# Performance work log

Measured on AMD Instinct MI355X. Metric: run time of the kernel, lower is better.

The kernel has to match this reference:

```python
import jax, jax.numpy as jnp
import numpy as np

B, HW, C = 32, 56, 128
WS, SS, NH = 7, 3, 4
HD = C // NH
SCALE = HD ** -0.5
NWIN = (HW // WS) ** 2  # 64 windows per image
N = WS * WS             # 49 tokens per window


def _build_constants():
    # relative position index [N, N] into flattened (13*13) bias table
    coords = np.stack(np.meshgrid(np.arange(WS), np.arange(WS), indexing='ij'))  # [2,7,7]
    cf = coords.reshape(2, -1)                       # [2,49]
    rel = cf[:, :, None] - cf[:, None, :]            # [2,49,49]
    rel = rel.transpose(1, 2, 0).copy()              # [49,49,2]
    rel[:, :, 0] += WS - 1
    rel[:, :, 1] += WS - 1
    rel[:, :, 0] *= 2 * WS - 1
    pos_index = rel.sum(-1)                          # [49,49]
    # shifted-window attention mask [nW, N, N]
    img = np.zeros((HW, HW))
    sl = (slice(0, -WS), slice(-WS, -SS), slice(-SS, None))
    cnt = 0
    for h in sl:
        for w in sl:
            img[h, w] = cnt
            cnt += 1
    mw = img.reshape(HW // WS, WS, HW // WS, WS).transpose(0, 2, 1, 3).reshape(NWIN, N)
    am = mw[:, None, :] - mw[:, :, None]             # unsqueeze(1) - unsqueeze(2)
    am = np.where(am != 0, -100.0, 0.0).astype(np.float32)
    return jnp.asarray(pos_index), jnp.asarray(am)

POS_INDEX, ATTN_MASK = _build_constants()


def _ln(x, w, b, eps=1e-5):
    mu = x.mean(-1, keepdims=True)
    var = ((x - mu) ** 2).mean(-1, keepdims=True)
    return (x - mu) * jax.lax.rsqrt(var + eps) * w + b


def setup_inputs() -> dict:
    key = jax.random.key(0)
    ks = jax.random.split(key, 10)
    s = 0.02
    return {
        'x': jax.random.normal(ks[0], (B, HW * HW, C), jnp.float32),
        'norm1_w': jnp.ones((C,), jnp.float32),
        'norm1_b': jnp.zeros((C,), jnp.float32),
        'qkv_w': jax.random.normal(ks[1], (C, 3 * C), jnp.float32) * s,
        'qkv_b': jax.random.normal(ks[2], (3 * C,), jnp.float32) * s,
        'proj_w': jax.random.normal(ks[3], (C, C), jnp.float32) * s,
        'proj_b': jax.random.normal(ks[4], (C,), jnp.float32) * s,
        'pos_bias_table': jax.random.normal(ks[5], (2 * WS - 1, 2 * WS - 1, NH), jnp.float32) * s,
        'mlp_w1': jax.random.normal(ks[6], (C, 4 * C), jnp.float32) * s,
        'mlp_b1': jnp.zeros((4 * C,), jnp.float32),
        'mlp_w2': jax.random.normal(ks[7], (4 * C, C), jnp.float32) * s,
        'mlp_b2': jnp.zeros((C,), jnp.float32),
        'norm2_w': jnp.ones((C,), jnp.float32),
        'norm2_b': jnp.zeros((C,), jnp.float32),
    }


def reference(x, norm1_w, norm1_b, qkv_w, qkv_b, proj_w, proj_b, pos_bias_table,
              mlp_w1, mlp_b1, mlp_w2, mlp_b2, norm2_w, norm2_b):
    G = HW // WS  # grid of windows per side
    Bw = B * NWIN
    shortcut = x
    y = _ln(x, norm1_w, norm1_b).reshape(B, HW, HW, C)
    # cyclic shift
    y = jnp.roll(y, (-SS, -SS), axis=(1, 2))
    # window partition -> [B*nW, 49, C]
    yw = y.reshape(B, G, WS, G, WS, C).transpose(0, 1, 3, 2, 4, 5).reshape(Bw, N, C)
    # qkv projection
    qkv = (yw @ qkv_w + qkv_b).reshape(Bw, N, 3, NH, HD).transpose(2, 0, 3, 1, 4)
    q, k, v = qkv[0] * SCALE, qkv[1], qkv[2]  # [Bw, NH, N, HD]
    attn = jnp.einsum('bhnd,bhmd->bhnm', q, k)
    # relative position bias [NH, N, N]
    bias = pos_bias_table.reshape(-1, NH)[POS_INDEX]  # [N,N,NH]
    attn = attn + bias.transpose(2, 0, 1)[None]
    # shift mask per window
    attn = attn.reshape(B, NWIN, NH, N, N) + ATTN_MASK[None, :, None]
    attn = jax.nn.softmax(attn.reshape(Bw, NH, N, N), axis=-1)
    out = jnp.einsum('bhnm,bhmd->bhnd', attn, v).transpose(0, 2, 1, 3).reshape(Bw, N, C)
    out = out @ proj_w + proj_b
    # window reverse
    out = out.reshape(B, G, G, WS, WS, C).transpose(0, 1, 3, 2, 4, 5).reshape(B, HW, HW, C)
    out = jnp.roll(out, (SS, SS), axis=(1, 2)).reshape(B, HW * HW, C)
    x = shortcut + out
    h = _ln(x, norm2_w, norm2_b)
    h = jax.nn.gelu(h @ mlp_w1 + mlp_b1, approximate=False) @ mlp_w2 + mlp_b2
    return x + h
```

## Files before the change

kernel.cpp:

```cpp
#include <hip/hip_runtime.h>
#include <hip/hip_bf16.h>

#define NTOK 100352
#define SCALE_Q 0.17677669529663687f

typedef __bf16 bf16x8 __attribute__((ext_vector_type(8)));
typedef float f32x4 __attribute__((ext_vector_type(4)));
struct bf2 { __hip_bfloat16 x, y; };
struct __align__(8) bh4 { __hip_bfloat16 a, b, c, d; };

__device__ __forceinline__ int wt_to_tok(int wt) {
  int w = wt / 49, n = wt - w * 49;
  int b = w >> 6, wi = w & 63;
  int gh = wi >> 3, gw = wi & 7;
  int r = n / 7, c = n - r * 7;
  int hs = gh * 7 + r + 3; if (hs >= 56) hs -= 56;
  int ws = gw * 7 + c + 3; if (ws >= 56) ws -= 56;
  return (b * 56 + hs) * 56 + ws;
}

__device__ __forceinline__ float gelu_fast(float v) {
  float y = 0.7978845608028654f * (v + 0.044715f * v * v * v);
  float ay = fabsf(y);
  float e = __expf(-2.0f * ay);
  float t = (1.0f - e) / (1.0f + e);
  t = copysignf(t, y);
  return 0.5f * v * (1.0f + t);
}

__global__ __launch_bounds__(256) void prep_all(const float* __restrict__ qkvw,
                                                const float* __restrict__ projw,
                                                const float* __restrict__ w1,
                                                const float* __restrict__ w2,
                                                __hip_bfloat16* __restrict__ dst) {
  int i = blockIdx.x * 256 + threadIdx.x;
  float v;
  if (i < 49152) { int n = i >> 7, k = i & 127; v = qkvw[k * 384 + n]; }
  else if (i < 65536) { int j = i - 49152; int n = j >> 7, k = j & 127; v = projw[k * 128 + n]; }
  else if (i < 131072) { int j = i - 65536; int n = j >> 7, k = j & 127; v = w1[k * 512 + n]; }
  else { int j = i - 131072; int n = j / 512, k = j - n * 512; v = w2[k * 128 + n]; }
  dst[i] = __float2bfloat16(v);
}

__global__ __launch_bounds__(256) void ln1_apply(const float* __restrict__ x,
                                                 const float* __restrict__ nw,
                                                 const float* __restrict__ nb,
                                                 __hip_bfloat16* __restrict__ xn) {
  int wt = blockIdx.x * 4 + (threadIdx.x >> 6);
  int lane = threadIdx.x & 63;
  int tok = wt_to_tok(wt);
  float2 v = *(const float2*)(x + (size_t)tok * 128 + lane * 2);
  float s = v.x + v.y, ss = v.x * v.x + v.y * v.y;
#pragma unroll
  for (int off = 32; off; off >>= 1) {
    s += __shfl_xor(s, off);
    ss += __shfl_xor(ss, off);
  }
  float mu = s * (1.0f / 128.0f);
  float rstd = rsqrtf(ss * (1.0f / 128.0f) - mu * mu + 1e-5f);
  float2 wv = *(const float2*)(nw + lane * 2);
  float2 bv = *(const float2*)(nb + lane * 2);
  bf2 o;
  o.x = __float2bfloat16((v.x - mu) * rstd * wv.x + bv.x);
  o.y = __float2bfloat16((v.y - mu) * rstd * wv.y + bv.y);
  *(bf2*)(xn + (size_t)wt * 128 + lane * 2) = o;
}

__global__ __launch_bounds__(256) void attn_mfma(const __hip_bfloat16* __restrict__ qkv,
                                                 const float* __restrict__ ptab,
                                                 __hip_bfloat16* __restrict__ attnout) {
  __shared__ __align__(16) char lds[4 * 12288];
  const int tid = threadIdx.x;
  const int lane = tid & 63, h = tid >> 6;
  const int w = blockIdx.x;
  const int wi = w & 63, gh = wi >> 3, gw = wi & 7;
  char* Pl = lds + h * 12288;
  char* VTl = Pl + 8192;
  const int lxi = lane & 15, lq = lane >> 4, lg4 = (lane >> 4) * 4;

  const __hip_bfloat16* base = qkv + (size_t)w * 49 * 384 + h * 32;
  __hip_bfloat16* op = attnout + (size_t)w * 49 * 128 + h * 32;

  bf16x8 qa[4], kb[4];
#pragma unroll
  for (int mi = 0; mi < 4; ++mi) {
    int t = mi * 16 + lxi; if (t > 48) t = 48;
    qa[mi] = *(const bf16x8*)(base + (size_t)t * 384 + lq * 8);
    kb[mi] = *(const bf16x8*)(base + (size_t)t * 384 + 128 + lq * 8);
  }
  {
    union { bf16x8 v; __hip_bfloat16 e[8]; } vv[4];
    const __hip_bfloat16* vp = base + (size_t)(lane < 49 ? lane : 0) * 384 + 256;
#pragma unroll
    for (int q = 0; q < 4; ++q) vv[q].v = *(const bf16x8*)(vp + q * 8);
    __hip_bfloat16 z = __float2bfloat16(0.0f);
#pragma unroll
    for (int q = 0; q < 4; ++q)
#pragma unroll
      for (int e = 0; e < 8; ++e) {
        int d = q * 8 + e;
        __hip_bfloat16 val = (lane < 49) ? vv[q].e[e] : z;
        *(__hip_bfloat16*)(VTl + d * 128 + ((lane * 2) ^ ((d & 7) << 4))) = val;
      }
  }

  f32x4 s[4][4] = {};
#pragma unroll
  for (int mi = 0; mi < 4; ++mi)
#pragma unroll
    for (int ni = 0; ni < 4; ++ni)
      s[mi][ni] = __builtin_amdgcn_mfma_f32_16x16x32_bf16(qa[mi], kb[ni], s[mi][ni], 0, 0, 0);

  int rj[4], cj[4], cntj[4], jbad[4];
#pragma unroll
  for (int ni = 0; ni < 4; ++ni) {
    int jc = ni * 16 + lxi;
    jbad[ni] = (jc > 48);
    int jj = jbad[ni] ? 48 : jc;
    rj[ni] = jj / 7; cj[ni] = jj - rj[ni] * 7;
    int hj = gh * 7 + rj[ni], wj = gw * 7 + cj[ni];
    cntj[ni] = (hj < 49 ? 0 : (hj < 53 ? 3 : 6)) + (wj < 49 ? 0 : (wj < 53 ? 1 : 2));
  }
#pragma unroll
  for (int mi = 0; mi < 4; ++mi)
#pragma unroll
    for (int j = 0; j < 4; ++j) {
      int i = mi * 16 + lg4 + j; if (i > 48) i = 48;
      int ri = i / 7, ci = i - ri * 7;
      int hi_ = gh * 7 + ri, wi_ = gw * 7 + ci;
      int cnti = (hi_ < 49 ? 0 : (hi_ < 53 ? 3 : 6)) + (wi_ < 49 ? 0 : (wi_ < 53 ? 1 : 2));
#pragma unroll
      for (int ni = 0; ni < 4; ++ni) {
        float b = ptab[((ri - rj[ni] + 6) * 13 + (ci - cj[ni] + 6)) * 4 + h];
        float val = s[mi][ni][j] * SCALE_Q + b;
        if (cnti != cntj[ni]) val -= 100.0f;
        if (jbad[ni]) val = -1e30f;
        s[mi][ni][j] = val;
      }
    }

#pragma unroll
  for (int mi = 0; mi < 4; ++mi)
#pragma unroll
    for (int j = 0; j < 4; ++j) {
      float m = fmaxf(fmaxf(s[mi][0][j], s[mi][1][j]), fmaxf(s[mi][2][j], s[mi][3][j]));
#pragma unroll
      for (int off = 8; off; off >>= 1) m = fmaxf(m, __shfl_xor(m, off));
      float e[4], sum = 0.0f;
#pragma unroll
      for (int ni = 0; ni < 4; ++ni) { e[ni] = __expf(s[mi][ni][j] - m); sum += e[ni]; }
#pragma unroll
      for (int off = 8; off; off >>= 1) sum += __shfl_xor(sum, off);
      float inv = 1.0f / sum;
#pragma unroll
      for (int ni = 0; ni < 4; ++ni) s[mi][ni][j] = e[ni] * inv;
    }

#pragma unroll
  for (int mi = 0; mi < 4; ++mi)
#pragma unroll
    for (int j = 0; j < 4; ++j) {
      int row = mi * 16 + lg4 + j;
      int sw = (row & 7) << 4;
      char* prow = Pl + row * 128;
#pragma unroll
      for (int ni = 0; ni < 4; ++ni)
        *(__hip_bfloat16*)(prow + (((ni * 16 + lxi) * 2) ^ sw)) =
            __float2bfloat16(s[mi][ni][j]);
    }

  __syncthreads();

  f32x4 o[4][2] = {};
#pragma unroll
  for (int ks = 0; ks < 2; ++ks) {
    bf16x8 pa[4], vb[2];
#pragma unroll
    for (int mi = 0; mi < 4; ++mi) {
      int row = mi * 16 + lxi;
      pa[mi] = *(const bf16x8*)(Pl + row * 128 + ((ks * 64 + lq * 16) ^ ((row & 7) << 4)));
    }
#pragma unroll
    for (int ni = 0; ni < 2; ++ni) {
      int row = ni * 16 + lxi;
      vb[ni] = *(const bf16x8*)(VTl + row * 128 + ((ks * 64 + lq * 16) ^ ((row & 7) << 4)));
    }
#pragma unroll
    for (int mi = 0; mi < 4; ++mi)
#pragma unroll
      for (int ni = 0; ni < 2; ++ni)
        o[mi][ni] = __builtin_amdgcn_mfma_f32_16x16x32_bf16(pa[mi], vb[ni], o[mi][ni], 0, 0, 0);
  }

#pragma unroll
  for (int mi = 0; mi < 4; ++mi)
#pragma unroll
    for (int j = 0; j < 4; ++j) {
      int q = mi * 16 + lg4 + j;
      if (q < 49) {
#pragma unroll
        for (int ni = 0; ni < 2; ++ni)
          op[(size_t)q * 128 + ni * 16 + lxi] = __float2bfloat16(o[mi][ni][j]);
      }
    }
}

template<int EPI>
__global__ __launch_bounds__(256) void gemm_mfma(
    const __hip_bfloat16* __restrict__ A, int lda, int NB,
    const __hip_bfloat16* __restrict__ Wt,
    const float* __restrict__ bias,
    void* __restrict__ outv, int ldo,
    __hip_bfloat16* __restrict__ out2,
    const float* __restrict__ nw, const float* __restrict__ nb,
    const float* __restrict__ resf, int K)
{
  __shared__ __align__(16) char AsB[128 * 256];
  __shared__ float redS[256], redQ[256];
  const int bid = blockIdx.x;
  const int xcd = bid & 7, tt = bid >> 3;
  const int nbk = tt % NB, mseq = tt / NB;
  const int m0 = (mseq * 8 + xcd) * 128, n0 = nbk * 128;
  const int tid = threadIdx.x;
  const int srow = tid >> 1;
  const int scol = (tid & 1) * 64;
  const int lane = tid & 63, wid = tid >> 6;
  const int wm = wid >> 1, wn = wid & 1;
  const int lrow = lane & 15, lq = lane >> 4;

  f32x4 acc[4][4] = {};

  for (int k0 = 0; k0 < K; k0 += 128) {
    {
      const char* ap = (const char*)A + ((size_t)(m0 + srow) * lda + k0 + scol) * 2;
      char* dst = AsB + srow * 256;
      int sw = (srow & 7) << 4;
#pragma unroll
      for (int t = 0; t < 8; ++t) {
        int4 raw = *(const int4*)(ap + t * 16);
        *(int4*)(dst + ((scol * 2 + t * 16) ^ sw)) = raw;
      }
    }
    __syncthreads();
#pragma unroll
    for (int ks = 0; ks < 4; ++ks) {
      int kb = ks * 64 + lq * 16;
      bf16x8 af[4], bfr[4];
#pragma unroll
      for (int mi = 0; mi < 4; ++mi) {
        int r = wm * 64 + mi * 16 + lrow;
        af[mi] = *(const bf16x8*)(AsB + r * 256 + (kb ^ ((r & 7) << 4)));
      }
#pragma unroll
      for (int ni = 0; ni < 4; ++ni) {
        int n = n0 + wn * 64 + ni * 16 + lrow;
        bfr[ni] = *(const bf16x8*)(Wt + (size_t)n * K + k0 + ks * 32 + lq * 8);
      }
#pragma unroll
      for (int mi = 0; mi < 4; ++mi)
#pragma unroll
        for (int ni = 0; ni < 4; ++ni)
          acc[mi][ni] = __builtin_amdgcn_mfma_f32_16x16x32_bf16(af[mi], bfr[ni], acc[mi][ni], 0, 0, 0);
    }
    __syncthreads();
  }

  float bv[4];
#pragma unroll
  for (int ni = 0; ni < 4; ++ni) bv[ni] = bias[n0 + wn * 64 + ni * 16 + lrow];

  if (EPI == 4) {
    __hip_bfloat16* x2 = (__hip_bfloat16*)outv;
    float nwc[4], nbc[4];
#pragma unroll
    for (int ni = 0; ni < 4; ++ni) {
      int colg = wn * 64 + ni * 16 + lrow;
      nwc[ni] = nw[colg]; nbc[ni] = nb[colg];
    }
    int toks[4][4];
#pragma unroll
    for (int mi = 0; mi < 4; ++mi)
#pragma unroll
      for (int j = 0; j < 4; ++j) {
        int row = wm * 64 + mi * 16 + lq * 4 + j;
        int tok = wt_to_tok(m0 + row);
        toks[mi][j] = tok;
        float s = 0.0f, ss = 0.0f;
#pragma unroll
        for (int ni = 0; ni < 4; ++ni) {
          int colg = wn * 64 + ni * 16 + lrow;
          float val = acc[mi][ni][j] + bv[ni] + resf[(size_t)tok * 128 + colg];
          x2[(size_t)tok * 128 + colg] = __float2bfloat16(val);
          acc[mi][ni][j] = val;
          s += val; ss += val * val;
        }
#pragma unroll
        for (int off = 8; off; off >>= 1) {
          s += __shfl_xor(s, off);
          ss += __shfl_xor(ss, off);
        }
        if (lrow == 0) { redS[row * 2 + wn] = s; redQ[row * 2 + wn] = ss; }
      }
    __syncthreads();
#pragma unroll
    for (int mi = 0; mi < 4; ++mi)
#pragma unroll
      for (int j = 0; j < 4; ++j) {
        int row = wm * 64 + mi * 16 + lq * 4 + j;
        float s = redS[row * 2] + redS[row * 2 + 1];
        float ss = redQ[row * 2] + redQ[row * 2 + 1];
        float mu = s * (1.0f / 128.0f);
        float rstd = rsqrtf(ss * (1.0f / 128.0f) - mu * mu + 1e-5f);
        int tok = toks[mi][j];
#pragma unroll
        for (int ni = 0; ni < 4; ++ni) {
          int colg = wn * 64 + ni * 16 + lrow;
          float xnv = (acc[mi][ni][j] - mu) * rstd * nwc[ni] + nbc[ni];
          out2[(size_t)tok * 128 + colg] = __float2bfloat16(xnv);
        }
      }
    return;
  }

#pragma unroll
  for (int mi = 0; mi < 4; ++mi) {
#pragma unroll
    for (int j = 0; j < 4; ++j) {
      int rowg = m0 + wm * 64 + mi * 16 + lq * 4 + j;
#pragma unroll
      for (int ni = 0; ni < 4; ++ni) {
        int colg = n0 + wn * 64 + ni * 16 + lrow;
        float val = acc[mi][ni][j] + bv[ni];
        ((__hip_bfloat16*)outv)[(size_t)rowg * ldo + colg] = __float2bfloat16(val);
      }
    }
  }
}

__global__ __launch_bounds__(256) void mlp_fused(
    const __hip_bfloat16* __restrict__ x2n,
    const __hip_bfloat16* __restrict__ w1T,
    const float* __restrict__ b1,
    const __hip_bfloat16* __restrict__ w2T,
    const float* __restrict__ b2,
    const __hip_bfloat16* __restrict__ x2,
    float* __restrict__ out)
{
  __shared__ __align__(16) char AsB[64 * 256];
  __shared__ __align__(16) char Hs[64 * 256];
  const int m0 = blockIdx.x * 64;
  const int tid = threadIdx.x;
  const int lane = tid & 63, wid = tid >> 6;
  const int wh = wid >> 1, wv = wid & 1;
  const int lrow = lane & 15, lq = lane >> 4;

  {
    const int srow = tid >> 2, scol = (tid & 3) * 32;
    const char* ap = (const char*)x2n + ((size_t)(m0 + srow) * 128 + scol) * 2;
    char* dst = AsB + srow * 256;
    int sw = (srow & 7) << 4;
#pragma unroll
    for (int t = 0; t < 4; ++t) {
      int4 raw = *(const int4*)(ap + t * 16);
      *(int4*)(dst + ((scol * 2 + t * 16) ^ sw)) = raw;
    }
  }
  __syncthreads();

  f32x4 oacc[2][4] = {};

  for (int c = 0; c < 4; ++c) {
    f32x4 hacc[4][2] = {};
#pragma unroll
    for (int ks = 0; ks < 4; ++ks) {
      int kb = ks * 64 + lq * 16;
      bf16x8 wf[4], afr[2];
#pragma unroll
      for (int mi = 0; mi < 4; ++mi) {
        int hd = c * 128 + wh * 64 + mi * 16 + lrow;
        wf[mi] = *(const bf16x8*)(w1T + (size_t)hd * 128 + ks * 32 + lq * 8);
      }
#pragma unroll
      for (int ni = 0; ni < 2; ++ni) {
        int r = wv * 32 + ni * 16 + lrow;
        afr[ni] = *(const bf16x8*)(AsB + r * 256 + (kb ^ ((r & 7) << 4)));
      }
#pragma unroll
      for (int mi = 0; mi < 4; ++mi)
#pragma unroll
        for (int ni = 0; ni < 2; ++ni)
          hacc[mi][ni] = __builtin_amdgcn_mfma_f32_16x16x32_bf16(wf[mi], afr[ni], hacc[mi][ni], 0, 0, 0);
    }
    __syncthreads();
#pragma unroll
    for (int mi = 0; mi < 4; ++mi) {
      int hdb = wh * 64 + mi * 16 + lq * 4;
      float b1v[4];
#pragma unroll
      for (int j = 0; j < 4; ++j) b1v[j] = b1[c * 128 + hdb + j];
#pragma unroll
      for (int ni = 0; ni < 2; ++ni) {
        int m_ = wv * 32 + ni * 16 + lrow;
        bh4 hv;
        hv.a = __float2bfloat16(gelu_fast(hacc[mi][ni][0] + b1v[0]));
        hv.b = __float2bfloat16(gelu_fast(hacc[mi][ni][1] + b1v[1]));
        hv.c = __float2bfloat16(gelu_fast(hacc[mi][ni][2] + b1v[2]));
        hv.d = __float2bfloat16(gelu_fast(hacc[mi][ni][3] + b1v[3]));
        *(bh4*)(Hs + m_ * 256 + ((hdb * 2) ^ ((m_ & 7) << 4))) = hv;
      }
    }
    __syncthreads();
#pragma unroll
    for (int ks = 0; ks < 4; ++ks) {
      int kb = ks * 64 + lq * 16;
      bf16x8 hf[2], w2f[4];
#pragma unroll
      for (int mi = 0; mi < 2; ++mi) {
        int r = wh * 32 + mi * 16 + lrow;
        hf[mi] = *(const bf16x8*)(Hs + r * 256 + (kb ^ ((r & 7) << 4)));
      }
#pragma unroll
      for (int ni = 0; ni < 4; ++ni) {
        int n = wv * 64 + ni * 16 + lrow;
        w2f[ni] = *(const bf16x8*)(w2T + (size_t)n * 512 + c * 128 + ks * 32 + lq * 8);
      }
#pragma unroll
      for (int mi = 0; mi < 2; ++mi)
#pragma unroll
        for (int ni = 0; ni < 4; ++ni)
          oacc[mi][ni] = __builtin_amdgcn_mfma_f32_16x16x32_bf16(hf[mi], w2f[ni], oacc[mi][ni], 0, 0, 0);
    }
  }

  float bv[4];
#pragma unroll
  for (int ni = 0; ni < 4; ++ni) bv[ni] = b2[wv * 64 + ni * 16 + lrow];
#pragma unroll
  for (int mi = 0; mi < 2; ++mi)
#pragma unroll
    for (int j = 0; j < 4; ++j) {
      int row = m0 + wh * 32 + mi * 16 + lq * 4 + j;
#pragma unroll
      for (int ni = 0; ni < 4; ++ni) {
        int col = wv * 64 + ni * 16 + lrow;
        float r = __bfloat162float(x2[(size_t)row * 128 + col]);
        out[(size_t)row * 128 + col] = oacc[mi][ni][j] + bv[ni] + r;
      }
    }
}

extern "C" void kernel_launch(void* const* d_in, const int* in_sizes, int n_in,
                              void* d_out, int out_size, void* d_ws, size_t ws_size,
                              hipStream_t stream) {
  (void)in_sizes; (void)n_in; (void)out_size; (void)ws_size;
  const float* x     = (const float*)d_in[0];
  const float* n1w   = (const float*)d_in[1];
  const float* n1b   = (const float*)d_in[2];
  const float* qkvw  = (const float*)d_in[3];
  const float* qkvb  = (const float*)d_in[4];
  const float* projw = (const float*)d_in[5];
  const float* projb = (const float*)d_in[6];
  const float* ptab  = (const float*)d_in[7];
  const float* w1    = (const float*)d_in[8];
  const float* b1    = (const float*)d_in[9];
  const float* w2    = (const float*)d_in[10];
  const float* b2    = (const float*)d_in[11];
  const float* n2w   = (const float*)d_in[12];
  const float* n2b   = (const float*)d_in[13];
  float* out = (float*)d_out;

  char* ws = (char*)d_ws;
  __hip_bfloat16* xn      = (__hip_bfloat16*)ws;
  __hip_bfloat16* qkv     = (__hip_bfloat16*)(ws + 25690112);
  __hip_bfloat16* attnout = (__hip_bfloat16*)(ws + 102760448);
  __hip_bfloat16* x2      = (__hip_bfloat16*)(ws + 128450560);
  __hip_bfloat16* x2n     = (__hip_bfloat16*)(ws + 154140672);
  __hip_bfloat16* wbase   = (__hip_bfloat16*)(ws + 179830784);
  __hip_bfloat16* qkvwT  = wbase;
  __hip_bfloat16* projwT = wbase + 49152;
  __hip_bfloat16* w1T    = wbase + 65536;
  __hip_bfloat16* w2T    = wbase + 131072;

  prep_all<<<768, 256, 0, stream>>>(qkvw, projw, w1, w2, wbase);
  ln1_apply<<<NTOK / 4, 256, 0, stream>>>(x, n1w, n1b, xn);
  gemm_mfma<0><<<784 * 3, 256, 0, stream>>>(xn, 128, 3, qkvwT, qkvb,
                                            qkv, 384, nullptr, nullptr, nullptr,
                                            nullptr, 128);
  attn_mfma<<<2048, 256, 0, stream>>>(qkv, ptab, attnout);
  gemm_mfma<4><<<784, 256, 0, stream>>>(attnout, 128, 1, projwT, projb,
                                        x2, 128, x2n, n2w, n2b, x, 128);
  mlp_fused<<<1568, 256, 0, stream>>>(x2n, w1T, b1, w2T, b2, x2, out);
}
```

Before: 271.4 us.

## Load GEMM A-operand fragments directly from global and double-buffer MLP hidden tile

In the projection GEMM, the A tile is no longer staged through swizzled shared memory. The K loop is also specialised to a single 128-wide step, so fragments come straight from global memory with no barriers. In the fused MLP, the shared-memory staging of the normalised input is removed and the hidden buffer is double-buffered, which drops one barrier per chunk. This reduces LDS traffic, sync overhead and shared-memory footprint, but adds redundant, less coalesced global reads that now rely on cache hits.

```diff
diff --git a/kernel.cpp b/kernel.cpp
--- a/kernel.cpp
+++ b/kernel.cpp
@@ -213,56 +213,41 @@
     void* __restrict__ outv, int ldo,
     __hip_bfloat16* __restrict__ out2,
     const float* __restrict__ nw, const float* __restrict__ nb,
-    const float* __restrict__ resf, int K)
+    const float* __restrict__ resf)
 {
-  __shared__ __align__(16) char AsB[128 * 256];
   __shared__ float redS[256], redQ[256];
   const int bid = blockIdx.x;
   const int xcd = bid & 7, tt = bid >> 3;
   const int nbk = tt % NB, mseq = tt / NB;
   const int m0 = (mseq * 8 + xcd) * 128, n0 = nbk * 128;
   const int tid = threadIdx.x;
-  const int srow = tid >> 1;
-  const int scol = (tid & 1) * 64;
   const int lane = tid & 63, wid = tid >> 6;
   const int wm = wid >> 1, wn = wid & 1;
   const int lrow = lane & 15, lq = lane >> 4;
 
   f32x4 acc[4][4] = {};
 
-  for (int k0 = 0; k0 < K; k0 += 128) {
-    {
-      const char* ap = (const char*)A + ((size_t)(m0 + srow) * lda + k0 + scol) * 2;
-      char* dst = AsB + srow * 256;
-      int sw = (srow & 7) << 4;
-#pragma unroll
-      for (int t = 0; t < 8; ++t) {
-        int4 raw = *(const int4*)(ap + t * 16);
-        *(int4*)(dst + ((scol * 2 + t * 16) ^ sw)) = raw;
-      }
-    }
-    __syncthreads();
-#pragma unroll
-    for (int ks = 0; ks < 4; ++ks) {
-      int kb = ks * 64 + lq * 16;
-      bf16x8 af[4], bfr[4];
-#pragma unroll
-      for (int mi = 0; mi < 4; ++mi) {
-        int r = wm * 64 + mi * 16 + lrow;
-        af[mi] = *(const bf16x8*)(AsB + r * 256 + (kb ^ ((r & 7) << 4)));
-      }
-#pragma unroll
-      for (int ni = 0; ni < 4; ++ni) {
-        int n = n0 + wn * 64 + ni * 16 + lrow;
-        bfr[ni] = *(const bf16x8*)(Wt + (size_t)n * K + k0 + ks * 32 + lq * 8);
-      }
-#pragma unroll
-      for (int mi = 0; mi < 4; ++mi)
-#pragma unroll
-        for (int ni = 0; ni < 4; ++ni)
-          acc[mi][ni] = __builtin_amdgcn_mfma_f32_16x16x32_bf16(af[mi], bfr[ni], acc[mi][ni], 0, 0, 0);
-    }
-    __syncthreads();
+  const __hip_bfloat16* arow[4];
+  const __hip_bfloat16* brow[4];
+#pragma unroll
+  for (int mi = 0; mi < 4; ++mi)
+    arow[mi] = A + (size_t)(m0 + wm * 64 + mi * 16 + lrow) * lda + lq * 8;
+#pragma unroll
+  for (int ni = 0; ni < 4; ++ni)
+    brow[ni] = Wt + (size_t)(n0 + wn * 64 + ni * 16 + lrow) * 128 + lq * 8;
+
+#pragma unroll
+  for (int ks = 0; ks < 4; ++ks) {
+    bf16x8 af[4], bfr[4];
+#pragma unroll
+    for (int mi = 0; mi < 4; ++mi) af[mi] = *(const bf16x8*)(arow[mi] + ks * 32);
+#pragma unroll
+    for (int ni = 0; ni < 4; ++ni) bfr[ni] = *(const bf16x8*)(brow[ni] + ks * 32);
+#pragma unroll
+    for (int mi = 0; mi < 4; ++mi)
+#pragma unroll
+      for (int ni = 0; ni < 4; ++ni)
+        acc[mi][ni] = __builtin_amdgcn_mfma_f32_16x16x32_bf16(af[mi], bfr[ni], acc[mi][ni], 0, 0, 0);
   }
 
   float bv[4];
@@ -346,34 +331,19 @@
     const __hip_bfloat16* __restrict__ x2,
     float* __restrict__ out)
 {
-  __shared__ __align__(16) char AsB[64 * 256];
-  __shared__ __align__(16) char Hs[64 * 256];
+  __shared__ __align__(16) char Hs[2][64 * 256];
   const int m0 = blockIdx.x * 64;
   const int tid = threadIdx.x;
   const int lane = tid & 63, wid = tid >> 6;
   const int wh = wid >> 1, wv = wid & 1;
   const int lrow = lane & 15, lq = lane >> 4;
 
-  {
-    const int srow = tid >> 2, scol = (tid & 3) * 32;
-    const char* ap = (const char*)x2n + ((size_t)(m0 + srow) * 128 + scol) * 2;
-    char* dst = AsB + srow * 256;
-    int sw = (srow & 7) << 4;
-#pragma unroll
-    for (int t = 0; t < 4; ++t) {
-      int4 raw = *(const int4*)(ap + t * 16);
-      *(int4*)(dst + ((scol * 2 + t * 16) ^ sw)) = raw;
-    }
-  }
-  __syncthreads();
-
   f32x4 oacc[2][4] = {};
 
   for (int c = 0; c < 4; ++c) {
     f32x4 hacc[4][2] = {};
 #pragma unroll
     for (int ks = 0; ks < 4; ++ks) {
-      int kb = ks * 64 + lq * 16;
       bf16x8 wf[4], afr[2];
 #pragma unroll
       for (int mi = 0; mi < 4; ++mi) {
@@ -382,8 +352,8 @@
       }
 #pragma unroll
       for (int ni = 0; ni < 2; ++ni) {
-        int r = wv * 32 + ni * 16 + lrow;
-        afr[ni] = *(const bf16x8*)(AsB + r * 256 + (kb ^ ((r & 7) << 4)));
+        int r = m0 + wv * 32 + ni * 16 + lrow;
+        afr[ni] = *(const bf16x8*)(x2n + (size_t)r * 128 + ks * 32 + lq * 8);
       }
 #pragma unroll
       for (int mi = 0; mi < 4; ++mi)
@@ -391,7 +361,7 @@
         for (int ni = 0; ni < 2; ++ni)
           hacc[mi][ni] = __builtin_amdgcn_mfma_f32_16x16x32_bf16(wf[mi], afr[ni], hacc[mi][ni], 0, 0, 0);
     }
-    __syncthreads();
+    char* hbuf = Hs[c & 1];
 #pragma unroll
     for (int mi = 0; mi < 4; ++mi) {
       int hdb = wh * 64 + mi * 16 + lq * 4;
@@ -406,7 +376,7 @@
         hv.b = __float2bfloat16(gelu_fast(hacc[mi][ni][1] + b1v[1]));
         hv.c = __float2bfloat16(gelu_fast(hacc[mi][ni][2] + b1v[2]));
         hv.d = __float2bfloat16(gelu_fast(hacc[mi][ni][3] + b1v[3]));
-        *(bh4*)(Hs + m_ * 256 + ((hdb * 2) ^ ((m_ & 7) << 4))) = hv;
+        *(bh4*)(hbuf + m_ * 256 + ((hdb * 2) ^ ((m_ & 7) << 4))) = hv;
       }
     }
     __syncthreads();
@@ -417,7 +387,7 @@
 #pragma unroll
       for (int mi = 0; mi < 2; ++mi) {
         int r = wh * 32 + mi * 16 + lrow;
-        hf[mi] = *(const bf16x8*)(Hs + r * 256 + (kb ^ ((r & 7) << 4)));
+        hf[mi] = *(const bf16x8*)(hbuf + r * 256 + (kb ^ ((r & 7) << 4)));
       }
 #pragma unroll
       for (int ni = 0; ni < 4; ++ni) {
@@ -485,9 +455,9 @@
   ln1_apply<<<NTOK / 4, 256, 0, stream>>>(x, n1w, n1b, xn);
   gemm_mfma<0><<<784 * 3, 256, 0, stream>>>(xn, 128, 3, qkvwT, qkvb,
                                             qkv, 384, nullptr, nullptr, nullptr,
-                                            nullptr, 128);
+                                            nullptr);
   attn_mfma<<<2048, 256, 0, stream>>>(qkv, ptab, attnout);
   gemm_mfma<4><<<784, 256, 0, stream>>>(attnout, 128, 1, projwT, projb,
-                                        x2, 128, x2n, n2w, n2b, x, 128);
+                                        x2, 128, x2n, n2w, n2b, x);
   mlp_fused<<<1568, 256, 0, stream>>>(x2n, w1T, b1, w2T, b2, x2, out);
 }
```

New measurement: 292.6 us. 1.08x slower.
